# Kernel tuning notes

Measured on AMD Instinct MI355X. Metric: run time of the kernel, lower is better.

## Reference

```python
import jax, jax.numpy as jnp
import numpy as np

B, N, C, G = 32, 1024, 64, 64

def setup_inputs() -> dict:
    key = jax.random.key(0)
    ks = jax.random.split(key, 8)
    return {
        "x": jax.random.normal(ks[0], (B, N, C), dtype=jnp.float32),
        "valid_len": jax.random.randint(ks[1], (B,), 0, N, dtype=jnp.int64) if jax.config.jax_enable_x64 else jax.random.randint(ks[1], (B,), 0, N, dtype=jnp.int32),
        "Wq": jax.random.normal(ks[2], (C, G), dtype=jnp.float32) * 0.1,
        "bq": jax.random.normal(ks[3], (G,), dtype=jnp.float32) * 0.1,
        "Wk": jax.random.normal(ks[4], (C, G), dtype=jnp.float32) * 0.1,
        "bk": jax.random.normal(ks[5], (G,), dtype=jnp.float32) * 0.1,
        "Wv": jax.random.normal(ks[6], (C, G), dtype=jnp.float32) * 0.1,
        "bv": jax.random.normal(ks[7], (G,), dtype=jnp.float32) * 0.1,
    }

def reference(x, valid_len, Wq, bq, Wk, bk, Wv, bv):
    # x: [B, N, C]; valid_len: [B] int (number of valid key positions per batch)
    q = x @ Wq + bq                                   # [B, N, G]
    k = x @ Wk + bk                                   # [B, N, G]
    v = x @ Wv + bv                                   # [B, N, G]
    scores = jnp.einsum('bnd,bmd->bnm', q, k)         # [B, N, N] (no 1/sqrt(d) scale)
    # mask: key positions >= valid_len[b] get -1e6 (matches original's -1000000.0 fill)
    col = jnp.arange(scores.shape[-1])
    mask = col[None, None, :] >= valid_len[:, None, None]
    scores = jnp.where(mask, jnp.float32(-1000000.0), scores)
    attn = jax.nn.softmax(scores, axis=-1)            # [B, N, N]
    return jnp.einsum('bnm,bmd->bnd', attn, v)        # [B, N, G]
```

## Files before the change

kernel.cpp:

```cpp
#include <hip/hip_runtime.h>
#include <stdint.h>


typedef __attribute__((ext_vector_type(4))) float    floatx4;
typedef __attribute__((ext_vector_type(8))) _Float16 halfx8;

static __device__ __forceinline__ unsigned short f2h(float f) {
    union { _Float16 h; unsigned short u; } v; v.h = (_Float16)f;
    return v.u;
}
static __device__ __forceinline__ float h2f(unsigned short u) {
    union { unsigned short u; _Float16 h; } v; v.u = u;
    return (float)v.h;
}

#define MFMA16(a, bb, c) __builtin_amdgcn_mfma_f32_16x16x32_f16((a), (bb), (c), 0, 0, 0)

__global__ __launch_bounds__(256, 2) void fused_attn_kernel(
    const float* __restrict__ x,
    const float* __restrict__ Wq, const float* __restrict__ bq,
    const float* __restrict__ Wk, const float* __restrict__ bk,
    const float* __restrict__ Wv, const float* __restrict__ bv,
    const int* __restrict__ valid_len, float* __restrict__ out)
{
    __shared__ __align__(16) unsigned short smem[28672];
    __shared__ int sched[32];

    const int Q_OFF = 0, XH_OFF = 4096, KL0_OFF = 8192, KL1_OFF = 12288,
              VS0_OFF = 16384, VS1_OFF = 20480, PS_OFF = 24576;

    const int tid  = threadIdx.x;
    const int blk  = blockIdx.x;
    const int lane = tid & 63;
    const int w    = tid >> 6;
    const int l15  = lane & 15;
    const int quad = lane >> 4;

    if (tid < 32) {
        int vlb = valid_len[tid];
        int ntb = (vlb == 0) ? 16 : ((vlb + 63) >> 6);
        int rank = 0;
        for (int b2 = 0; b2 < 32; ++b2) {
            int vl2 = valid_len[b2];
            int nt2 = (vl2 == 0) ? 16 : ((vl2 + 63) >> 6);
            rank += (nt2 > ntb) || (nt2 == ntb && b2 < tid);
        }
        sched[rank] = tid;
    }
    __syncthreads();

    const int hv   = (blk < 256);
    const int b    = hv ? sched[blk >> 4] : sched[31 - ((blk - 256) >> 4)];
    const int n0   = (blk & 15) * 64;
    const int row0 = b * 1024 + n0;

    const int xsl  = XH_OFF + w * 1024;
    const int fidx0 = l15 * 64 + (((0 + quad) ^ (l15 & 7)) * 8);
    const int fidx1 = l15 * 64 + (((4 + quad) ^ (l15 & 7)) * 8);
    const int rl   = lane >> 2;
    const int c8a  = 2 * (lane & 3);
    const int c8b  = 2 * (lane & 3) + 1;
    const int sidx_a = rl * 64 + ((c8a ^ (rl & 7)) * 8);
    const int sidx_b = rl * 64 + ((c8b ^ (rl & 7)) * 8);

    const int vl    = valid_len[b];
    const int nt    = (vl == 0) ? 16 : ((vl + 63) >> 6);
    const int fullt = vl >> 6;

    {
        const float* xrow = x + (size_t)(row0 + w * 16) * 64;
#pragma unroll
        for (int i = 0; i < 2; ++i) {
            int c8 = (i == 0) ? c8a : c8b;
            int sidx = (i == 0) ? sidx_a : sidx_b;
            const float4* gp = (const float4*)(xrow + rl * 64 + c8 * 8);
            float4 f0 = gp[0], f1 = gp[1];
            float fv[8] = { f0.x, f0.y, f0.z, f0.w, f1.x, f1.y, f1.z, f1.w };
            __align__(16) unsigned short thi[8], tlo[8];
#pragma unroll
            for (int j = 0; j < 8; ++j) {
                unsigned short hi = f2h(fv[j]);
                thi[j] = hi;
                tlo[j] = f2h(fv[j] - h2f(hi));
            }
            *(uint4*)&smem[xsl + sidx]                = *(uint4*)thi;
            *(uint4*)&smem[VS0_OFF + w * 1024 + sidx] = *(uint4*)tlo;
        }
    }
    {
        int g = tid & 63, ci = tid >> 6;
#pragma unroll
        for (int j = 0; j < 16; ++j) {
            int c = ci * 16 + j;
            int idx = g * 64 + (((c >> 3) ^ (g & 7)) * 8) + (c & 7);
            float fq = Wq[c * 64 + g];
            unsigned short qhi = f2h(fq);
            smem[KL0_OFF + idx] = qhi;
            smem[KL1_OFF + idx] = f2h(fq - h2f(qhi));
            smem[VS1_OFF + idx] = f2h(Wk[c * 64 + g]);
            smem[PS_OFF  + idx] = f2h(Wv[c * 64 + g]);
        }
    }
    __syncthreads();

    halfx8 wkf0[4], wkf1[4], wvf0[4], wvf1[4];
#pragma unroll
    for (int gs = 0; gs < 4; ++gs) {
        int brow = gs * 16 + l15;
        int b0 = brow * 64 + (((0 + quad) ^ (brow & 7)) * 8);
        int b1 = brow * 64 + (((4 + quad) ^ (brow & 7)) * 8);
        wkf0[gs] = *(const halfx8*)&smem[VS1_OFF + b0];
        wkf1[gs] = *(const halfx8*)&smem[VS1_OFF + b1];
        wvf0[gs] = *(const halfx8*)&smem[PS_OFF + b0];
        wvf1[gs] = *(const halfx8*)&smem[PS_OFF + b1];
    }

    {
        halfx8 ah0 = *(const halfx8*)&smem[xsl + fidx0];
        halfx8 ah1 = *(const halfx8*)&smem[xsl + fidx1];
        halfx8 al0 = *(const halfx8*)&smem[VS0_OFF + w * 1024 + fidx0];
        halfx8 al1 = *(const halfx8*)&smem[VS0_OFF + w * 1024 + fidx1];
#pragma unroll
        for (int gs = 0; gs < 4; ++gs) {
            int brow = gs * 16 + l15;
            float bb = bq[gs * 16 + l15];
            floatx4 acc = { bb, bb, bb, bb };
            int b0 = brow * 64 + (((0 + quad) ^ (brow & 7)) * 8);
            int b1 = brow * 64 + (((4 + quad) ^ (brow & 7)) * 8);
            halfx8 bh0 = *(const halfx8*)&smem[KL0_OFF + b0];
            halfx8 bh1 = *(const halfx8*)&smem[KL0_OFF + b1];
            halfx8 bl0 = *(const halfx8*)&smem[KL1_OFF + b0];
            halfx8 bl1 = *(const halfx8*)&smem[KL1_OFF + b1];
            acc = MFMA16(ah0, bh0, acc);
            acc = MFMA16(ah1, bh1, acc);
            acc = MFMA16(ah0, bl0, acc);
            acc = MFMA16(ah1, bl1, acc);
            acc = MFMA16(al0, bh0, acc);
            acc = MFMA16(al1, bh1, acc);
            int c8 = gs * 2 + (l15 >> 3);
#pragma unroll
            for (int r = 0; r < 4; ++r) {
                int row = w * 16 + quad * 4 + r;
                smem[Q_OFF + row * 64 + ((c8 ^ (row & 7)) * 8) + (l15 & 7)] = f2h(acc[r]);
            }
        }
    }
    const int arow = w * 16 + l15;
    halfx8 aq0 = *(const halfx8*)&smem[Q_OFF + arow * 64 + (((0 + quad) ^ (arow & 7)) * 8)];
    halfx8 aq1 = *(const halfx8*)&smem[Q_OFF + arow * 64 + (((4 + quad) ^ (arow & 7)) * 8)];

    {
        const float* xrow = x + (size_t)(b * 1024 + w * 16) * 64;
#pragma unroll
        for (int i = 0; i < 2; ++i) {
            int c8 = (i == 0) ? c8a : c8b;
            int sidx = (i == 0) ? sidx_a : sidx_b;
            const float4* gp = (const float4*)(xrow + rl * 64 + c8 * 8);
            float4 f0 = gp[0], f1 = gp[1];
            __align__(16) unsigned short thi[8] = {
                f2h(f0.x), f2h(f0.y), f2h(f0.z), f2h(f0.w),
                f2h(f1.x), f2h(f1.y), f2h(f1.z), f2h(f1.w) };
            *(uint4*)&smem[xsl + sidx] = *(uint4*)thi;
        }
    }
    __syncthreads();

    {
        halfx8 kxh0 = *(const halfx8*)&smem[xsl + fidx0];
        halfx8 kxh1 = *(const halfx8*)&smem[xsl + fidx1];
#pragma unroll
        for (int gs = 0; gs < 4; ++gs) {
            float bbk = bk[gs * 16 + l15];
            float bbv = bv[gs * 16 + l15];
            floatx4 kacc = { bbk, bbk, bbk, bbk };
            floatx4 vacc = { bbv, bbv, bbv, bbv };
            kacc = MFMA16(kxh0, wkf0[gs], kacc);
            kacc = MFMA16(kxh1, wkf1[gs], kacc);
            vacc = MFMA16(kxh0, wvf0[gs], vacc);
            vacc = MFMA16(kxh1, wvf1[gs], vacc);
            int c8 = gs * 2 + (l15 >> 3);
            int g  = gs * 16 + l15;
#pragma unroll
            for (int r = 0; r < 4; ++r) {
                int key = w * 16 + quad * 4 + r;
                smem[KL0_OFF + key * 64 + ((c8 ^ (key & 7)) * 8) + (l15 & 7)] = f2h(kacc[r]);
                smem[VS0_OFF + g * 64 + (((key >> 3) ^ (g & 7)) * 8) + (key & 7)] = f2h(vacc[r]);
            }
        }
    }

    float m_r[4]    = { -INFINITY, -INFINITY, -INFINITY, -INFINITY };
    float l_lane[4] = { 0.f, 0.f, 0.f, 0.f };
    floatx4 o[4] = { {0,0,0,0}, {0,0,0,0}, {0,0,0,0}, {0,0,0,0} };

    for (int t = 0; t < nt; ++t) {
        bool pre = (t + 1) < nt;
        float4 pfa0, pfa1, pfb0, pfb1;
        if (pre) {
            const float* xrow = x + (size_t)(b * 1024 + (t + 1) * 64 + w * 16) * 64;
            pfa0 = ((const float4*)(xrow + rl * 64 + c8a * 8))[0];
            pfa1 = ((const float4*)(xrow + rl * 64 + c8a * 8))[1];
            pfb0 = ((const float4*)(xrow + rl * 64 + c8b * 8))[0];
            pfb1 = ((const float4*)(xrow + rl * 64 + c8b * 8))[1];
        }
        __syncthreads();

        if (pre) {
            __align__(16) unsigned short ta[8] = {
                f2h(pfa0.x), f2h(pfa0.y), f2h(pfa0.z), f2h(pfa0.w),
                f2h(pfa1.x), f2h(pfa1.y), f2h(pfa1.z), f2h(pfa1.w) };
            __align__(16) unsigned short tb[8] = {
                f2h(pfb0.x), f2h(pfb0.y), f2h(pfb0.z), f2h(pfb0.w),
                f2h(pfb1.x), f2h(pfb1.y), f2h(pfb1.z), f2h(pfb1.w) };
            *(uint4*)&smem[xsl + sidx_a] = *(uint4*)ta;
            *(uint4*)&smem[xsl + sidx_b] = *(uint4*)tb;
            halfx8 kxh0 = *(const halfx8*)&smem[xsl + fidx0];
            halfx8 kxh1 = *(const halfx8*)&smem[xsl + fidx1];
            const int KLn = ((t + 1) & 1) ? KL1_OFF : KL0_OFF;
            const int VSn = ((t + 1) & 1) ? VS1_OFF : VS0_OFF;
#pragma unroll
            for (int gs = 0; gs < 4; ++gs) {
                float bbk = bk[gs * 16 + l15];
                float bbv = bv[gs * 16 + l15];
                floatx4 kacc = { bbk, bbk, bbk, bbk };
                floatx4 vacc = { bbv, bbv, bbv, bbv };
                kacc = MFMA16(kxh0, wkf0[gs], kacc);
                kacc = MFMA16(kxh1, wkf1[gs], kacc);
                vacc = MFMA16(kxh0, wvf0[gs], vacc);
                vacc = MFMA16(kxh1, wvf1[gs], vacc);
                int c8 = gs * 2 + (l15 >> 3);
                int g  = gs * 16 + l15;
#pragma unroll
                for (int r = 0; r < 4; ++r) {
                    int key = w * 16 + quad * 4 + r;
                    smem[KLn + key * 64 + ((c8 ^ (key & 7)) * 8) + (l15 & 7)] = f2h(kacc[r]);
                    smem[VSn + g * 64 + (((key >> 3) ^ (g & 7)) * 8) + (key & 7)] = f2h(vacc[r]);
                }
            }
        }

        const int KLc = (t & 1) ? KL1_OFF : KL0_OFF;
        const int VSc = (t & 1) ? VS1_OFF : VS0_OFF;

        floatx4 s[4];
#pragma unroll
        for (int sub = 0; sub < 4; ++sub) {
            int krow = sub * 16 + l15;
            halfx8 bk0 = *(const halfx8*)&smem[KLc + krow * 64 + (((0 + quad) ^ (krow & 7)) * 8)];
            halfx8 bk1 = *(const halfx8*)&smem[KLc + krow * 64 + (((4 + quad) ^ (krow & 7)) * 8)];
            floatx4 acc = { 0, 0, 0, 0 };
            acc = MFMA16(aq0, bk0, acc);
            acc = MFMA16(aq1, bk1, acc);
            s[sub] = acc;
        }
        if (t >= fullt) {
#pragma unroll
            for (int sub = 0; sub < 4; ++sub) {
                int key = t * 64 + sub * 16 + l15;
                if (key >= vl) { s[sub][0] = -1e6f; s[sub][1] = -1e6f; s[sub][2] = -1e6f; s[sub][3] = -1e6f; }
            }
        }

        float p[4][4];
        float alpha[4];
#pragma unroll
        for (int r = 0; r < 4; ++r) {
            float mx = fmaxf(fmaxf(s[0][r], s[1][r]), fmaxf(s[2][r], s[3][r]));
#pragma unroll
            for (int off = 1; off < 16; off <<= 1)
                mx = fmaxf(mx, __shfl_xor(mx, off, 64));
            float mnew = fmaxf(m_r[r], mx);
            alpha[r] = __expf(m_r[r] - mnew);
            float psum = 0.f;
#pragma unroll
            for (int sub = 0; sub < 4; ++sub) {
                float pv = __expf(s[sub][r] - mnew);
                p[sub][r] = pv;
                psum += pv;
            }
            l_lane[r] = l_lane[r] * alpha[r] + psum;
            m_r[r] = mnew;
        }
#pragma unroll
        for (int gs = 0; gs < 4; ++gs) {
            o[gs][0] *= alpha[0]; o[gs][1] *= alpha[1];
            o[gs][2] *= alpha[2]; o[gs][3] *= alpha[3];
        }

        unsigned short* psw = &smem[PS_OFF + w * 1024];
#pragma unroll
        for (int sub = 0; sub < 4; ++sub) {
            int c8 = sub * 2 + (l15 >> 3);
#pragma unroll
            for (int r = 0; r < 4; ++r) {
                int row = quad * 4 + r;
                psw[row * 64 + ((c8 ^ (row & 7)) * 8) + (l15 & 7)] = f2h(p[sub][r]);
            }
        }
        halfx8 ap0 = *(const halfx8*)&psw[fidx0];
        halfx8 ap1 = *(const halfx8*)&psw[fidx1];

#pragma unroll
        for (int gs = 0; gs < 4; ++gs) {
            int grow = gs * 16 + l15;
            halfx8 bv0 = *(const halfx8*)&smem[VSc + grow * 64 + (((0 + quad) ^ (grow & 7)) * 8)];
            halfx8 bv1 = *(const halfx8*)&smem[VSc + grow * 64 + (((4 + quad) ^ (grow & 7)) * 8)];
            o[gs] = MFMA16(ap0, bv0, o[gs]);
            o[gs] = MFMA16(ap1, bv1, o[gs]);
        }
    }

    float l[4];
#pragma unroll
    for (int r = 0; r < 4; ++r) {
        float ss = l_lane[r];
#pragma unroll
        for (int off = 1; off < 16; off <<= 1)
            ss += __shfl_xor(ss, off, 64);
        l[r] = ss;
    }
#pragma unroll
    for (int gs = 0; gs < 4; ++gs) {
#pragma unroll
        for (int r = 0; r < 4; ++r) {
            int row = row0 + w * 16 + quad * 4 + r;
            out[row * 64 + gs * 16 + l15] = o[gs][r] / l[r];
        }
    }
}

extern "C" void kernel_launch(void* const* d_in, const int* in_sizes, int n_in,
                              void* d_out, int out_size, void* d_ws, size_t ws_size,
                              hipStream_t stream) {
    const float* x    = (const float*)d_in[0];
    const int*   vlen = (const int*)  d_in[1];
    const float* Wq   = (const float*)d_in[2];
    const float* bq   = (const float*)d_in[3];
    const float* Wk   = (const float*)d_in[4];
    const float* bk   = (const float*)d_in[5];
    const float* Wv   = (const float*)d_in[6];
    const float* bv   = (const float*)d_in[7];
    float* out = (float*)d_out;

    fused_attn_kernel<<<512, 256, 0, stream>>>(
        x, Wq, bq, Wk, bk, Wv, bv, vlen, out);
}
```

Before: 107.4 us.

## Split fused attention into projection kernel and pipelined attention kernel

Splits the single fused kernel into two. The first computes the Q/K/V projections once per row tile and writes fp16 swizzled tiles to workspace. The second streams those K/V tiles into LDS with async global-to-LDS loads through a triple buffer. This removes the per-block recomputation of K/V projections that the fused version likely did, at the cost of an extra launch and a workspace round trip. It falls back to the old fused kernel if the workspace is too small.

```diff
diff --git a/kernel.cpp b/kernel.cpp
--- a/kernel.cpp
+++ b/kernel.cpp
@@ -16,7 +16,323 @@
 
 #define MFMA16(a, bb, c) __builtin_amdgcn_mfma_f32_16x16x32_f16((a), (bb), (c), 0, 0, 0)
 
-__global__ __launch_bounds__(256, 2) void fused_attn_kernel(
+#define GLD_LDS16(g, l) __builtin_amdgcn_global_load_lds(                  \
+    (const __attribute__((address_space(1))) void*)(g),                    \
+    (__attribute__((address_space(3))) void*)(l), 16, 0, 0)
+
+__global__ __launch_bounds__(256, 2) void proj_kernel(
+    const float* __restrict__ x,
+    const float* __restrict__ Wq, const float* __restrict__ bq,
+    const float* __restrict__ Wk, const float* __restrict__ bk,
+    const float* __restrict__ Wv, const float* __restrict__ bv,
+    unsigned short* __restrict__ qimg,
+    unsigned short* __restrict__ kimg,
+    unsigned short* __restrict__ vimg)
+{
+    __shared__ __align__(16) unsigned short sm[24576];
+    const int XH = 0, XL = 4096, WQH = 8192, WQL = 12288, WKH = 16384, WVH = 20480;
+
+    const int tid  = threadIdx.x;
+    const int blk  = blockIdx.x;
+    const int lane = tid & 63;
+    const int w    = tid >> 6;
+    const int l15  = lane & 15;
+    const int quad = lane >> 4;
+    const int rl   = lane >> 2;
+    const int c8a  = 2 * (lane & 3);
+    const int c8b  = c8a + 1;
+    const int sidx_a = rl * 64 + ((c8a ^ (rl & 7)) * 8);
+    const int sidx_b = rl * 64 + ((c8b ^ (rl & 7)) * 8);
+
+    {
+        const float* xrow = x + (size_t)(blk * 64 + w * 16) * 64;
+#pragma unroll
+        for (int i = 0; i < 2; ++i) {
+            int c8   = (i == 0) ? c8a : c8b;
+            int sidx = (i == 0) ? sidx_a : sidx_b;
+            const float4* gp = (const float4*)(xrow + rl * 64 + c8 * 8);
+            float4 f0 = gp[0], f1 = gp[1];
+            float fv[8] = { f0.x, f0.y, f0.z, f0.w, f1.x, f1.y, f1.z, f1.w };
+            __align__(16) unsigned short thi[8], tlo[8];
+#pragma unroll
+            for (int j = 0; j < 8; ++j) {
+                unsigned short hi = f2h(fv[j]);
+                thi[j] = hi;
+                tlo[j] = f2h(fv[j] - h2f(hi));
+            }
+            *(uint4*)&sm[XH + w * 1024 + sidx] = *(uint4*)thi;
+            *(uint4*)&sm[XL + w * 1024 + sidx] = *(uint4*)tlo;
+        }
+    }
+    {
+        int g = tid & 63, ci = tid >> 6;
+#pragma unroll
+        for (int j = 0; j < 16; ++j) {
+            int c = ci * 16 + j;
+            int idx = g * 64 + (((c >> 3) ^ (g & 7)) * 8) + (c & 7);
+            float fq = Wq[c * 64 + g];
+            unsigned short qhi = f2h(fq);
+            sm[WQH + idx] = qhi;
+            sm[WQL + idx] = f2h(fq - h2f(qhi));
+            sm[WKH + idx] = f2h(Wk[c * 64 + g]);
+            sm[WVH + idx] = f2h(Wv[c * 64 + g]);
+        }
+    }
+    __syncthreads();
+
+    const int fidx0 = l15 * 64 + (((0 + quad) ^ (l15 & 7)) * 8);
+    const int fidx1 = l15 * 64 + (((4 + quad) ^ (l15 & 7)) * 8);
+    halfx8 ah0 = *(const halfx8*)&sm[XH + w * 1024 + fidx0];
+    halfx8 ah1 = *(const halfx8*)&sm[XH + w * 1024 + fidx1];
+    halfx8 al0 = *(const halfx8*)&sm[XL + w * 1024 + fidx0];
+    halfx8 al1 = *(const halfx8*)&sm[XL + w * 1024 + fidx1];
+
+    floatx4 vacc[4];
+#pragma unroll
+    for (int gs = 0; gs < 4; ++gs) {
+        int brow = gs * 16 + l15;
+        int b0 = brow * 64 + (((0 + quad) ^ (brow & 7)) * 8);
+        int b1 = brow * 64 + (((4 + quad) ^ (brow & 7)) * 8);
+        halfx8 bh0 = *(const halfx8*)&sm[WQH + b0];
+        halfx8 bh1 = *(const halfx8*)&sm[WQH + b1];
+        halfx8 bl0 = *(const halfx8*)&sm[WQL + b0];
+        halfx8 bl1 = *(const halfx8*)&sm[WQL + b1];
+        halfx8 wk0 = *(const halfx8*)&sm[WKH + b0];
+        halfx8 wk1 = *(const halfx8*)&sm[WKH + b1];
+        halfx8 wv0 = *(const halfx8*)&sm[WVH + b0];
+        halfx8 wv1 = *(const halfx8*)&sm[WVH + b1];
+
+        float bbq = bq[gs * 16 + l15];
+        floatx4 qa = { bbq, bbq, bbq, bbq };
+        qa = MFMA16(ah0, bh0, qa);
+        qa = MFMA16(ah1, bh1, qa);
+        qa = MFMA16(ah0, bl0, qa);
+        qa = MFMA16(ah1, bl1, qa);
+        qa = MFMA16(al0, bh0, qa);
+        qa = MFMA16(al1, bh1, qa);
+
+        float bbk = bk[gs * 16 + l15];
+        float bbv = bv[gs * 16 + l15];
+        floatx4 ka = { bbk, bbk, bbk, bbk };
+        floatx4 va = { bbv, bbv, bbv, bbv };
+        ka = MFMA16(ah0, wk0, ka);
+        ka = MFMA16(ah1, wk1, ka);
+        va = MFMA16(ah0, wv0, va);
+        va = MFMA16(ah1, wv1, va);
+        vacc[gs] = va;
+
+        int c8 = gs * 2 + (l15 >> 3);
+#pragma unroll
+        for (int r = 0; r < 4; ++r) {
+            int row = w * 16 + quad * 4 + r;
+            int idx = row * 64 + ((c8 ^ (row & 7)) * 8) + (l15 & 7);
+            sm[XH + idx] = f2h(qa[r]);
+            sm[XL + idx] = f2h(ka[r]);
+        }
+    }
+    __syncthreads();
+#pragma unroll
+    for (int gs = 0; gs < 4; ++gs) {
+        int g = gs * 16 + l15;
+#pragma unroll
+        for (int r = 0; r < 4; ++r) {
+            int key = w * 16 + quad * 4 + r;
+            sm[WQH + g * 64 + (((key >> 3) ^ (g & 7)) * 8) + (key & 7)] = f2h(vacc[gs][r]);
+        }
+    }
+    __syncthreads();
+
+    {
+        const size_t tb = (size_t)blk * 4096;
+#pragma unroll
+        for (int i = 0; i < 2; ++i) {
+            int ci = i * 256 + tid;
+            *(uint4*)&qimg[tb + ci * 8] = *(const uint4*)&sm[XH  + ci * 8];
+            *(uint4*)&kimg[tb + ci * 8] = *(const uint4*)&sm[XL  + ci * 8];
+            *(uint4*)&vimg[tb + ci * 8] = *(const uint4*)&sm[WQH + ci * 8];
+        }
+    }
+}
+
+__global__ __launch_bounds__(256, 2) void attn_kernel(
+    const unsigned short* __restrict__ qimg,
+    const unsigned short* __restrict__ kimg,
+    const unsigned short* __restrict__ vimg,
+    const int* __restrict__ valid_len, float* __restrict__ out)
+{
+    __shared__ __align__(16) unsigned short smem[28672];
+    __shared__ int sched[32];
+    const int VSB = 12288, PS_OFF = 24576;
+
+    const int tid  = threadIdx.x;
+    const int blk  = blockIdx.x;
+    const int lane = tid & 63;
+    const int w    = tid >> 6;
+    const int l15  = lane & 15;
+    const int quad = lane >> 4;
+
+    if (tid < 32) {
+        int vlb = valid_len[tid];
+        int ntb = (vlb == 0) ? 16 : ((vlb + 63) >> 6);
+        int rank = 0;
+        for (int b2 = 0; b2 < 32; ++b2) {
+            int vl2 = valid_len[b2];
+            int nt2 = (vl2 == 0) ? 16 : ((vl2 + 63) >> 6);
+            rank += (nt2 > ntb) || (nt2 == ntb && b2 < tid);
+        }
+        sched[rank] = tid;
+    }
+    __syncthreads();
+
+    const int b    = (blk < 256) ? sched[blk >> 4] : sched[31 - ((blk - 256) >> 4)];
+    const int qt   = blk & 15;
+    const int row0 = b * 1024 + qt * 64;
+
+    const int vl    = valid_len[b];
+    const int nt    = (vl == 0) ? 16 : ((vl + 63) >> 6);
+    const int fullt = vl >> 6;
+
+    const int arow = w * 16 + l15;
+    const unsigned short* qb = qimg + (size_t)(b * 16 + qt) * 4096;
+    halfx8 aq0 = *(const halfx8*)&qb[arow * 64 + (((0 + quad) ^ (arow & 7)) * 8)];
+    halfx8 aq1 = *(const halfx8*)&qb[arow * 64 + (((4 + quad) ^ (arow & 7)) * 8)];
+
+    const char* kbase = (const char*)kimg + (size_t)b * 131072 + w * 2048 + lane * 16;
+    const char* vbase = (const char*)vimg + (size_t)b * 131072 + w * 2048 + lane * 16;
+
+    {
+        unsigned short* kd = &smem[w * 1024];
+        unsigned short* vd = &smem[VSB + w * 1024];
+        GLD_LDS16(kbase,        kd);
+        GLD_LDS16(kbase + 1024, kd + 512);
+        GLD_LDS16(vbase,        vd);
+        GLD_LDS16(vbase + 1024, vd + 512);
+        if (nt > 1) {
+            unsigned short* kd1 = &smem[4096 + w * 1024];
+            unsigned short* vd1 = &smem[VSB + 4096 + w * 1024];
+            GLD_LDS16(kbase + 8192,        kd1);
+            GLD_LDS16(kbase + 8192 + 1024, kd1 + 512);
+            GLD_LDS16(vbase + 8192,        vd1);
+            GLD_LDS16(vbase + 8192 + 1024, vd1 + 512);
+        }
+    }
+
+    float m_r[4]    = { -INFINITY, -INFINITY, -INFINITY, -INFINITY };
+    float l_lane[4] = { 0.f, 0.f, 0.f, 0.f };
+    floatx4 o[4] = { {0,0,0,0}, {0,0,0,0}, {0,0,0,0}, {0,0,0,0} };
+
+    int cur = 0;
+    for (int t = 0; t < nt; ++t) {
+        if (t + 1 < nt) asm volatile("s_waitcnt vmcnt(4)" ::: "memory");
+        else            asm volatile("s_waitcnt vmcnt(0)" ::: "memory");
+        __builtin_amdgcn_s_barrier();
+        asm volatile("" ::: "memory");
+
+        if (t + 2 < nt) {
+            int nb = cur + 2; if (nb >= 3) nb -= 3;
+            unsigned short* kd = &smem[nb * 4096 + w * 1024];
+            unsigned short* vd = &smem[VSB + nb * 4096 + w * 1024];
+            const char* kt2 = kbase + (size_t)(t + 2) * 8192;
+            const char* vt2 = vbase + (size_t)(t + 2) * 8192;
+            GLD_LDS16(kt2,        kd);
+            GLD_LDS16(kt2 + 1024, kd + 512);
+            GLD_LDS16(vt2,        vd);
+            GLD_LDS16(vt2 + 1024, vd + 512);
+        }
+
+        const int KLc = cur * 4096;
+        const int VSc = VSB + cur * 4096;
+
+        floatx4 s[4];
+#pragma unroll
+        for (int sub = 0; sub < 4; ++sub) {
+            int krow = sub * 16 + l15;
+            halfx8 bk0 = *(const halfx8*)&smem[KLc + krow * 64 + (((0 + quad) ^ (krow & 7)) * 8)];
+            halfx8 bk1 = *(const halfx8*)&smem[KLc + krow * 64 + (((4 + quad) ^ (krow & 7)) * 8)];
+            floatx4 acc = { 0, 0, 0, 0 };
+            acc = MFMA16(aq0, bk0, acc);
+            acc = MFMA16(aq1, bk1, acc);
+            s[sub] = acc;
+        }
+        if (t >= fullt) {
+#pragma unroll
+            for (int sub = 0; sub < 4; ++sub) {
+                int key = t * 64 + sub * 16 + l15;
+                if (key >= vl) { s[sub][0] = -1e6f; s[sub][1] = -1e6f; s[sub][2] = -1e6f; s[sub][3] = -1e6f; }
+            }
+        }
+
+        float p[4][4];
+        float alpha[4];
+#pragma unroll
+        for (int r = 0; r < 4; ++r) {
+            float mx = fmaxf(fmaxf(s[0][r], s[1][r]), fmaxf(s[2][r], s[3][r]));
+#pragma unroll
+            for (int off = 1; off < 16; off <<= 1)
+                mx = fmaxf(mx, __shfl_xor(mx, off, 64));
+            float mnew = fmaxf(m_r[r], mx);
+            alpha[r] = __expf(m_r[r] - mnew);
+            float psum = 0.f;
+#pragma unroll
+            for (int sub = 0; sub < 4; ++sub) {
+                float pv = __expf(s[sub][r] - mnew);
+                p[sub][r] = pv;
+                psum += pv;
+            }
+            l_lane[r] = l_lane[r] * alpha[r] + psum;
+            m_r[r] = mnew;
+        }
+#pragma unroll
+        for (int gs = 0; gs < 4; ++gs) {
+            o[gs][0] *= alpha[0]; o[gs][1] *= alpha[1];
+            o[gs][2] *= alpha[2]; o[gs][3] *= alpha[3];
+        }
+
+        unsigned short* psw = &smem[PS_OFF + w * 1024];
+#pragma unroll
+        for (int sub = 0; sub < 4; ++sub) {
+            int c8 = sub * 2 + (l15 >> 3);
+#pragma unroll
+            for (int r = 0; r < 4; ++r) {
+                int row = quad * 4 + r;
+                psw[row * 64 + ((c8 ^ (row & 7)) * 8) + (l15 & 7)] = f2h(p[sub][r]);
+            }
+        }
+        halfx8 ap0 = *(const halfx8*)&psw[l15 * 64 + (((0 + quad) ^ (l15 & 7)) * 8)];
+        halfx8 ap1 = *(const halfx8*)&psw[l15 * 64 + (((4 + quad) ^ (l15 & 7)) * 8)];
+
+#pragma unroll
+        for (int gs = 0; gs < 4; ++gs) {
+            int grow = gs * 16 + l15;
+            halfx8 bv0 = *(const halfx8*)&smem[VSc + grow * 64 + (((0 + quad) ^ (grow & 7)) * 8)];
+            halfx8 bv1 = *(const halfx8*)&smem[VSc + grow * 64 + (((4 + quad) ^ (grow & 7)) * 8)];
+            o[gs] = MFMA16(ap0, bv0, o[gs]);
+            o[gs] = MFMA16(ap1, bv1, o[gs]);
+        }
+
+        cur = (cur == 2) ? 0 : cur + 1;
+    }
+
+    float l[4];
+#pragma unroll
+    for (int r = 0; r < 4; ++r) {
+        float ss = l_lane[r];
+#pragma unroll
+        for (int off = 1; off < 16; off <<= 1)
+            ss += __shfl_xor(ss, off, 64);
+        l[r] = ss;
+    }
+#pragma unroll
+    for (int gs = 0; gs < 4; ++gs) {
+#pragma unroll
+        for (int r = 0; r < 4; ++r) {
+            int row = row0 + w * 16 + quad * 4 + r;
+            out[row * 64 + gs * 16 + l15] = o[gs][r] / l[r];
+        }
+    }
+}
+
+__global__ __launch_bounds__(256, 2) void fused_attn_fallback(
     const float* __restrict__ x,
     const float* __restrict__ Wq, const float* __restrict__ bq,
     const float* __restrict__ Wk, const float* __restrict__ bk,
@@ -342,6 +658,18 @@
     const float* bv   = (const float*)d_in[7];
     float* out = (float*)d_out;
 
-    fused_attn_kernel<<<512, 256, 0, stream>>>(
-        x, Wq, bq, Wk, bk, Wv, bv, vlen, out);
+    const size_t IMG_SHORTS = (size_t)32 * 16 * 4096;
+    const size_t NEED = 3 * IMG_SHORTS * sizeof(unsigned short);
+
+    if (ws_size >= NEED) {
+        unsigned short* qimg = (unsigned short*)d_ws;
+        unsigned short* kimg = qimg + IMG_SHORTS;
+        unsigned short* vimg = kimg + IMG_SHORTS;
+        proj_kernel<<<512, 256, 0, stream>>>(x, Wq, bq, Wk, bk, Wv, bv,
+                                             qimg, kimg, vimg);
+        attn_kernel<<<512, 256, 0, stream>>>(qimg, kimg, vimg, vlen, out);
+    } else {
+        fused_attn_fallback<<<512, 256, 0, stream>>>(
+            x, Wq, bq, Wk, bk, Wv, bv, vlen, out);
+    }
 }
```

New measurement: 106.1 us. Within noise of the previous version (-1.3%).
